# Optimization experiments

Hardware: AMD Instinct MI355X
Metric: run time of the kernel (lower is better)

## Reference

```python
import jax, jax.numpy as jnp
import numpy as np

N_NODES = 100000


def gcn_conv(x, edge_src, edge_dst, W, b):
    # PyG GCNConv: h = x @ W; add self-loops; symmetric normalization; scatter-add; + bias
    n = x.shape[0]
    h = x @ W  # [N, out]
    loop = jnp.arange(n, dtype=edge_src.dtype)
    src = jnp.concatenate([edge_src, loop])
    dst = jnp.concatenate([edge_dst, loop])
    deg = jax.ops.segment_sum(jnp.ones_like(dst, dtype=h.dtype), dst, num_segments=n)
    dinv = jnp.where(deg > 0, jax.lax.rsqrt(deg), 0.0)
    norm = dinv[src] * dinv[dst]  # [E+N]
    msg = h[src] * norm[:, None]  # gather + scale
    out = jax.ops.segment_sum(msg, dst, num_segments=n)  # scatter-add
    return out + b


def setup_inputs() -> dict:
    key = jax.random.key(0)
    ks = jax.random.split(key, 12)
    F_in, H, H2, C = 128, 64, 32, 2
    x = jax.random.normal(ks[0], (N_NODES, F_in), dtype=jnp.float32)
    edge_index = jax.random.randint(ks[1], (2, 3200000), 0, N_NODES, dtype=jnp.int64)
    def glorot(k, shape):
        lim = float(np.sqrt(6.0 / (shape[0] + shape[1])))
        return jax.random.uniform(k, shape, jnp.float32, -lim, lim)
    return {
        "x": x,
        "edge_index": edge_index,
        "W1": glorot(ks[2], (F_in, H)), "b1": jnp.zeros((H,), jnp.float32),
        "W2": glorot(ks[3], (H, H)), "b2": jnp.zeros((H,), jnp.float32),
        "Wl1": glorot(ks[4], (H, H2)), "bl1": jnp.zeros((H2,), jnp.float32),
        "Wl2": glorot(ks[5], (H2, C)), "bl2": jnp.zeros((C,), jnp.float32),
    }


def reference(x, edge_index, W1, b1, W2, b2, Wl1, bl1, Wl2, bl2):
    src, dst = edge_index[0], edge_index[1]
    h = gcn_conv(x, src, dst, W1, b1)
    h = jax.nn.relu(h)
    # dropout is identity in eval mode (training=self.training)
    h = gcn_conv(h, src, dst, W2, b2)
    h = h @ Wl1 + bl1
    h = h @ Wl2 + bl2
    return jax.nn.softmax(h, axis=0)
```

## Files before the change

### kernel.cpp

```cpp
#include <hip/hip_runtime.h>

#define F_IN 128
#define NBMAX 512
#define TILE1 8192
#define CAP2 10240

typedef __attribute__((ext_vector_type(8))) short short8;
typedef __attribute__((ext_vector_type(4))) float f32x4;
typedef __attribute__((ext_vector_type(2))) float f32x2;

__device__ __forceinline__ unsigned short f2bf(float f) {
    unsigned u = __float_as_uint(f);
    u += 0x7fffu + ((u >> 16) & 1u);
    return (unsigned short)(u >> 16);
}
__device__ __forceinline__ float bflo(unsigned u) { return __uint_as_float(u << 16); }
__device__ __forceinline__ float bfhi(unsigned u) { return __uint_as_float(u & 0xffff0000u); }

__device__ __forceinline__ unsigned char f2fp8(float f) {
    return (unsigned char)(__builtin_amdgcn_cvt_pk_fp8_f32(f, f, 0, false) & 0xff);
}

__global__ __launch_bounds__(512) void k_cnt(const int* __restrict__ dst, int E,
                                             int* __restrict__ bcnt, int nb) {
    __shared__ int h[NBMAX];
    int t = threadIdx.x;
    for (int i = t; i < nb; i += 512) h[i] = 0;
    __syncthreads();
    int base = blockIdx.x * TILE1;
    int end = min(base + TILE1, E);
    for (int i = base + t; i < end; i += 512)
        atomicAdd(&h[dst[i] >> 8], 1);
    __syncthreads();
    for (int i = t; i < nb; i += 512)
        if (h[i]) atomicAdd(&bcnt[i], h[i]);
}

__global__ __launch_bounds__(512) void k_bscan1(const int* __restrict__ bcnt,
                                                int* __restrict__ boff,
                                                int* __restrict__ cursor, int nb) {
    __shared__ int part[512];
    int t = threadIdx.x;
    int v = (t < nb) ? bcnt[t] : 0;
    part[t] = v;
    __syncthreads();
    for (int d = 1; d < 512; d <<= 1) {
        int u = (t >= d) ? part[t - d] : 0;
        __syncthreads();
        part[t] += u;
        __syncthreads();
    }
    if (t < nb) { boff[t] = part[t] - v; cursor[t] = part[t] - v; }
    if (t == 511) boff[nb] = part[511];
}

__global__ __launch_bounds__(1024) void k_part1(const int* __restrict__ src,
                                                const int* __restrict__ dst,
                                                int* __restrict__ cursor,
                                                unsigned* __restrict__ ebuf,
                                                int E, int nb) {
    __shared__ unsigned staged[TILE1];
    __shared__ unsigned short sbuck[TILE1];
    __shared__ int hist[NBMAX], lbase[NBMAX], lcur[NBMAX], gbase[NBMAX];
    int t = threadIdx.x;
    for (int i = t; i < nb; i += 1024) hist[i] = 0;
    __syncthreads();
    int base = blockIdx.x * TILE1;
    int end = min(base + TILE1, E);
    for (int i = base + t; i < end; i += 1024)
        atomicAdd(&hist[dst[i] >> 8], 1);
    __syncthreads();
    if (t < 64) {
        int carry = 0;
        for (int c = 0; c < (nb + 63) / 64; ++c) {
            int idx = c * 64 + t;
            int v = (idx < nb) ? hist[idx] : 0;
            int inc = v;
            for (int d = 1; d < 64; d <<= 1) {
                int u = __shfl_up(inc, d, 64);
                if (t >= d) inc += u;
            }
            if (idx < nb) { int ex = carry + inc - v; lbase[idx] = ex; lcur[idx] = ex; }
            carry += __shfl(inc, 63, 64);
        }
    }
    __syncthreads();
    for (int i = t; i < nb; i += 1024)
        gbase[i] = hist[i] ? atomicAdd(&cursor[i], hist[i]) : 0;
    for (int i = base + t; i < end; i += 1024) {
        int d = dst[i];
        int b = d >> 8;
        int r = atomicAdd(&lcur[b], 1);
        staged[r] = ((unsigned)src[i] << 8) | (unsigned)(d & 255);
        sbuck[r] = (unsigned short)b;
    }
    __syncthreads();
    int cnt = end - base;
    for (int i = t; i < cnt; i += 1024) {
        int b = sbuck[i];
        ebuf[gbase[b] + (i - lbase[b])] = staged[i];
    }
}

__global__ __launch_bounds__(1024) void k_part2(const unsigned* __restrict__ ebuf,
                                                const int* __restrict__ boff,
                                                int* __restrict__ csr,
                                                int* __restrict__ offs,
                                                float* __restrict__ dinv, int n) {
    __shared__ unsigned staged[CAP2];
    __shared__ int hist[256], lcur[256];
    int t = threadIdx.x;
    int b = blockIdx.x;
    int beg = boff[b], end = boff[b + 1];
    int cnt = end - beg;
    if (t < 256) hist[t] = 0;
    __syncthreads();
    for (int i = beg + t; i < end; i += 1024)
        atomicAdd(&hist[ebuf[i] & 255u], 1);
    __syncthreads();
    if (t < 64) {
        int carry = 0;
        for (int c = 0; c < 4; ++c) {
            int idx = c * 64 + t;
            int v = hist[idx];
            int inc = v;
            for (int d = 1; d < 64; d <<= 1) {
                int u = __shfl_up(inc, d, 64);
                if (t >= d) inc += u;
            }
            int ex = carry + inc - v;
            lcur[idx] = ex;
            int node = b * 256 + idx;
            if (node <= n) offs[node] = beg + ex;
            if (node < n) dinv[node] = rsqrtf((float)(v + 1));
            carry += __shfl(inc, 63, 64);
        }
    }
    __syncthreads();
    if (cnt <= CAP2) {
        for (int i = beg + t; i < end; i += 1024) {
            unsigned e = ebuf[i];
            int r = atomicAdd(&lcur[(int)(e & 255u)], 1);
            staged[r] = e >> 8;
        }
        __syncthreads();
        for (int i = t; i < cnt; i += 1024)
            csr[beg + i] = (int)staged[i];
    } else {
        for (int i = beg + t; i < end; i += 1024) {
            unsigned e = ebuf[i];
            int r = atomicAdd(&lcur[(int)(e & 255u)], 1);
            csr[beg + r] = (int)(e >> 8);
        }
    }
}

__global__ __launch_bounds__(256) void k_wfold(const float* __restrict__ W2,
                                               const float* __restrict__ b2,
                                               const float* __restrict__ Wl1,
                                               const float* __restrict__ bl1,
                                               const float* __restrict__ Wl2,
                                               const float* __restrict__ bl2,
                                               float* __restrict__ Wfold,
                                               float* __restrict__ bconst) {
    __shared__ float Wc[64][2];
    __shared__ float bc0[2];
    int t = threadIdx.x;
    if (t < 128) {
        int k = t >> 1, c = t & 1;
        float s = 0.f;
        for (int m = 0; m < 32; ++m) s += Wl1[k * 32 + m] * Wl2[m * 2 + c];
        Wc[k][c] = s;
    } else if (t < 130) {
        int c = t - 128;
        float s = bl2[c];
        for (int m = 0; m < 32; ++m) s += bl1[m] * Wl2[m * 2 + c];
        bc0[c] = s;
    }
    __syncthreads();
    if (t < 128) {
        int k = t >> 1, c = t & 1;
        float s = 0.f;
        for (int j = 0; j < 64; ++j) s += W2[k * 64 + j] * Wc[j][c];
        Wfold[k * 2 + c] = s;
    } else if (t < 130) {
        int c = t - 128;
        float s = bc0[c];
        for (int j = 0; j < 64; ++j) s += b2[j] * Wc[j][c];
        bconst[c] = s;
    }
}

template<int K, bool INBF16>
__global__ __launch_bounds__(256) void k_gemm_mfma(const void* __restrict__ Xv,
                                                   const float* __restrict__ W,
                                                   const float* __restrict__ dinv,
                                                   unsigned* __restrict__ G, int n) {
    constexpr int AST = K + 8;
    __shared__ unsigned short A_lds[64 * AST];
    __shared__ unsigned short Wt_lds[64 * AST];
    __shared__ unsigned char C8[64 * 68];
    int t = threadIdx.x;
    int base = blockIdx.x * 64;

    for (int idx = t; idx < K * 64; idx += 256) {
        int k = idx >> 6, nn = idx & 63;
        Wt_lds[nn * AST + k] = f2bf(W[idx]);
    }
    if (!INBF16) {
        const f32x4* X4 = (const f32x4*)Xv;
        constexpr int F4 = K / 4;
        for (int idx = t; idx < 64 * F4; idx += 256) {
            int row = idx / F4, c4 = idx % F4;
            f32x4 f = {0.f, 0.f, 0.f, 0.f};
            if (base + row < n) f = X4[(size_t)base * F4 + idx];
            unsigned p0 = (unsigned)f2bf(f.x) | ((unsigned)f2bf(f.y) << 16);
            unsigned p1 = (unsigned)f2bf(f.z) | ((unsigned)f2bf(f.w) << 16);
            *(uint2*)&A_lds[row * AST + c4 * 4] = make_uint2(p0, p1);
        }
    } else {
        const unsigned* H32 = (const unsigned*)Xv;
        constexpr int U2 = K / 2;
        for (int idx = t; idx < 64 * U2; idx += 256) {
            int row = idx / U2, c2 = idx % U2;
            unsigned u = 0;
            if (base + row < n) u = H32[(size_t)base * U2 + idx];
            *(unsigned*)&A_lds[row * AST + c2 * 2] = u;
        }
    }
    __syncthreads();

    int lane = t & 63, w = t >> 6;
    int q = lane >> 4, m = lane & 15;
    f32x4 acc0 = {0,0,0,0}, acc1 = {0,0,0,0}, acc2 = {0,0,0,0}, acc3 = {0,0,0,0};
    const unsigned short* arow = &A_lds[(16 * w + m) * AST + q * 8];
#pragma unroll
    for (int s = 0; s < K / 32; ++s) {
        short8 a  = *(const short8*)(arow + s * 32);
        short8 w0 = *(const short8*)&Wt_lds[ m       * AST + s * 32 + q * 8];
        short8 w1 = *(const short8*)&Wt_lds[(16 + m) * AST + s * 32 + q * 8];
        short8 w2 = *(const short8*)&Wt_lds[(32 + m) * AST + s * 32 + q * 8];
        short8 w3 = *(const short8*)&Wt_lds[(48 + m) * AST + s * 32 + q * 8];
        acc0 = __builtin_amdgcn_mfma_f32_16x16x32_bf16(a, w0, acc0, 0, 0, 0);
        acc1 = __builtin_amdgcn_mfma_f32_16x16x32_bf16(a, w1, acc1, 0, 0, 0);
        acc2 = __builtin_amdgcn_mfma_f32_16x16x32_bf16(a, w2, acc2, 0, 0, 0);
        acc3 = __builtin_amdgcn_mfma_f32_16x16x32_bf16(a, w3, acc3, 0, 0, 0);
    }
    float dv[4];
#pragma unroll
    for (int r = 0; r < 4; ++r) {
        int node = base + 16 * w + q * 4 + r;
        dv[r] = (node < n) ? dinv[node] : 0.f;
    }
#pragma unroll
    for (int r = 0; r < 4; ++r) {
        int row = 16 * w + q * 4 + r;
        C8[row * 68 + m]      = f2fp8(acc0[r] * dv[r]);
        C8[row * 68 + 16 + m] = f2fp8(acc1[r] * dv[r]);
        C8[row * 68 + 32 + m] = f2fp8(acc2[r] * dv[r]);
        C8[row * 68 + 48 + m] = f2fp8(acc3[r] * dv[r]);
    }
    __syncthreads();
    for (int idx = t; idx < 1024; idx += 256) {
        int row = idx >> 4, c4 = idx & 15;
        int node = base + row;
        if (node < n) G[(size_t)node * 16 + c4] = *(const unsigned*)&C8[row * 68 + c4 * 4];
    }
}

__global__ __launch_bounds__(256) void k_gfold(const int* __restrict__ csr,
                                               const int* __restrict__ offs,
                                               const unsigned* __restrict__ G,
                                               const float* __restrict__ dinv,
                                               const float* __restrict__ bias,
                                               const float* __restrict__ Wfold,
                                               float2* __restrict__ P, int n) {
    int w = (blockIdx.x * 256 + threadIdx.x) >> 6;
    if (w >= n) return;
    int lane = threadIdx.x & 63;
    int g = lane >> 4, sl = lane & 15;
    float a0 = 0.f, a1 = 0.f, a2 = 0.f, a3 = 0.f;
    {
        unsigned u = G[(size_t)w * 16 + sl];
        if (g != 0) u = 0u;
        f32x2 lo = __builtin_amdgcn_cvt_pk_f32_fp8((int)u, false);
        f32x2 hi = __builtin_amdgcn_cvt_pk_f32_fp8((int)u, true);
        a0 += lo.x; a1 += lo.y; a2 += hi.x; a3 += hi.y;
    }
    int beg = offs[w], end = offs[w + 1];
    int e = beg;
    int c0 = 0, c1 = 0, c2 = 0, c3 = 0;
    if (e + 16 <= end) {
        c0 = csr[e + g];      c1 = csr[e + 4 + g];
        c2 = csr[e + 8 + g];  c3 = csr[e + 12 + g];
    }
    while (e + 16 <= end) {
        unsigned u0 = G[(size_t)c0 * 16 + sl];
        unsigned u1 = G[(size_t)c1 * 16 + sl];
        unsigned u2 = G[(size_t)c2 * 16 + sl];
        unsigned u3 = G[(size_t)c3 * 16 + sl];
        int ne = e + 16;
        if (ne + 16 <= end) {
            c0 = csr[ne + g];      c1 = csr[ne + 4 + g];
            c2 = csr[ne + 8 + g];  c3 = csr[ne + 12 + g];
        }
        f32x2 p;
        p = __builtin_amdgcn_cvt_pk_f32_fp8((int)u0, false); a0 += p.x; a1 += p.y;
        p = __builtin_amdgcn_cvt_pk_f32_fp8((int)u0, true);  a2 += p.x; a3 += p.y;
        p = __builtin_amdgcn_cvt_pk_f32_fp8((int)u1, false); a0 += p.x; a1 += p.y;
        p = __builtin_amdgcn_cvt_pk_f32_fp8((int)u1, true);  a2 += p.x; a3 += p.y;
        p = __builtin_amdgcn_cvt_pk_f32_fp8((int)u2, false); a0 += p.x; a1 += p.y;
        p = __builtin_amdgcn_cvt_pk_f32_fp8((int)u2, true);  a2 += p.x; a3 += p.y;
        p = __builtin_amdgcn_cvt_pk_f32_fp8((int)u3, false); a0 += p.x; a1 += p.y;
        p = __builtin_amdgcn_cvt_pk_f32_fp8((int)u3, true);  a2 += p.x; a3 += p.y;
        e = ne;
    }
    for (; e + 4 <= end; e += 4) {
        int c = csr[e + g];
        unsigned u = G[(size_t)c * 16 + sl];
        f32x2 lo = __builtin_amdgcn_cvt_pk_f32_fp8((int)u, false);
        f32x2 hi = __builtin_amdgcn_cvt_pk_f32_fp8((int)u, true);
        a0 += lo.x; a1 += lo.y; a2 += hi.x; a3 += hi.y;
    }
    int rem = end - e;
    if (rem > 0) {
        int c = csr[(g < rem) ? (e + g) : e];
        unsigned u = G[(size_t)c * 16 + sl];
        if (g >= rem) u = 0u;
        f32x2 lo = __builtin_amdgcn_cvt_pk_f32_fp8((int)u, false);
        f32x2 hi = __builtin_amdgcn_cvt_pk_f32_fp8((int)u, true);
        a0 += lo.x; a1 += lo.y; a2 += hi.x; a3 += hi.y;
    }
    a0 += __shfl_xor(a0, 16, 64); a1 += __shfl_xor(a1, 16, 64);
    a2 += __shfl_xor(a2, 16, 64); a3 += __shfl_xor(a3, 16, 64);
    a0 += __shfl_xor(a0, 32, 64); a1 += __shfl_xor(a1, 32, 64);
    a2 += __shfl_xor(a2, 32, 64); a3 += __shfl_xor(a3, 32, 64);
    float d = dinv[w];
    float4 bb = ((const float4*)bias)[sl];
    float v0 = fmaxf(fmaf(a0, d, bb.x), 0.f);
    float v1 = fmaxf(fmaf(a1, d, bb.y), 0.f);
    float v2 = fmaxf(fmaf(a2, d, bb.z), 0.f);
    float v3 = fmaxf(fmaf(a3, d, bb.w), 0.f);
    float4 wa = ((const float4*)Wfold)[2 * sl];
    float4 wb = ((const float4*)Wfold)[2 * sl + 1];
    float px = v0 * wa.x + v1 * wa.z + v2 * wb.x + v3 * wb.z;
    float py = v0 * wa.y + v1 * wa.w + v2 * wb.y + v3 * wb.w;
    px += __shfl_xor(px, 1, 64); py += __shfl_xor(py, 1, 64);
    px += __shfl_xor(px, 2, 64); py += __shfl_xor(py, 2, 64);
    px += __shfl_xor(px, 4, 64); py += __shfl_xor(py, 4, 64);
    px += __shfl_xor(px, 8, 64); py += __shfl_xor(py, 8, 64);
    if (lane == 0) P[w] = make_float2(px * d, py * d);
}

__global__ __launch_bounds__(256) void k_gather2(const int* __restrict__ csr,
                                                 const int* __restrict__ offs,
                                                 const float2* __restrict__ P,
                                                 const float* __restrict__ dinv,
                                                 const float* __restrict__ bconst,
                                                 float* __restrict__ logits, int n) {
    int w = (blockIdx.x * 256 + threadIdx.x) >> 4;
    if (w >= n) return;
    int sl = threadIdx.x & 15;
    int beg = offs[w], end = offs[w + 1];
    float ax = 0.f, ay = 0.f;
    for (int i = beg + sl; i < end; i += 16) {
        float2 p = P[csr[i]];
        ax += p.x; ay += p.y;
    }
    ax += __shfl_xor(ax, 1, 64); ay += __shfl_xor(ay, 1, 64);
    ax += __shfl_xor(ax, 2, 64); ay += __shfl_xor(ay, 2, 64);
    ax += __shfl_xor(ax, 4, 64); ay += __shfl_xor(ay, 4, 64);
    ax += __shfl_xor(ax, 8, 64); ay += __shfl_xor(ay, 8, 64);
    if (sl == 0) {
        float2 self = P[w];
        float d = dinv[w];
        logits[w * 2]     = d * (self.x + ax) + bconst[0];
        logits[w * 2 + 1] = d * (self.y + ay) + bconst[1];
    }
}

__global__ __launch_bounds__(256) void k_sm_part(const float* __restrict__ logits,
                                                 float4* __restrict__ partials, int n) {
    __shared__ float r0[256], r1[256];
    int t = threadIdx.x;
    int i = blockIdx.x * 256 + t;
    float l0 = -3.4e38f, l1 = -3.4e38f;
    if (i < n) { l0 = logits[i * 2]; l1 = logits[i * 2 + 1]; }
    r0[t] = l0; r1[t] = l1;
    __syncthreads();
    for (int s = 128; s > 0; s >>= 1) {
        if (t < s) { r0[t] = fmaxf(r0[t], r0[t + s]); r1[t] = fmaxf(r1[t], r1[t + s]); }
        __syncthreads();
    }
    float m0 = r0[0], m1 = r1[0];
    __syncthreads();
    r0[t] = (i < n) ? __expf(l0 - m0) : 0.f;
    r1[t] = (i < n) ? __expf(l1 - m1) : 0.f;
    __syncthreads();
    for (int s = 128; s > 0; s >>= 1) {
        if (t < s) { r0[t] += r0[t + s]; r1[t] += r1[t + s]; }
        __syncthreads();
    }
    if (t == 0) partials[blockIdx.x] = make_float4(m0, r0[0], m1, r1[0]);
}

__global__ __launch_bounds__(512) void k_sm_comb(const float4* __restrict__ partials,
                                                 float4* __restrict__ glob, int nb) {
    __shared__ float m0s[512], s0s[512], m1s[512], s1s[512];
    int t = threadIdx.x;
    float4 p = (t < nb) ? partials[t] : make_float4(-3.4e38f, 0.f, -3.4e38f, 0.f);
    m0s[t] = p.x; m1s[t] = p.z;
    __syncthreads();
    for (int s = 256; s > 0; s >>= 1) {
        if (t < s) { m0s[t] = fmaxf(m0s[t], m0s[t + s]); m1s[t] = fmaxf(m1s[t], m1s[t + s]); }
        __syncthreads();
    }
    float M0 = m0s[0], M1 = m1s[0];
    s0s[t] = (t < nb) ? p.y * __expf(p.x - M0) : 0.f;
    s1s[t] = (t < nb) ? p.w * __expf(p.z - M1) : 0.f;
    __syncthreads();
    for (int s = 256; s > 0; s >>= 1) {
        if (t < s) { s0s[t] += s0s[t + s]; s1s[t] += s1s[t + s]; }
        __syncthreads();
    }
    if (t == 0) *glob = make_float4(M0, 1.f / s0s[0], M1, 1.f / s1s[0]);
}

__global__ __launch_bounds__(256) void k_sm_final(const float* __restrict__ logits,
                                                  const float4* __restrict__ glob,
                                                  float* __restrict__ out, int n) {
    int i = blockIdx.x * 256 + threadIdx.x;
    if (i < n) {
        float4 g = *glob;
        out[i * 2]     = __expf(logits[i * 2]     - g.x) * g.y;
        out[i * 2 + 1] = __expf(logits[i * 2 + 1] - g.z) * g.w;
    }
}

extern "C" void kernel_launch(void* const* d_in, const int* in_sizes, int n_in,
                              void* d_out, int out_size, void* d_ws, size_t ws_size,
                              hipStream_t stream) {
    const float* x   = (const float*)d_in[0];
    const int*   ei  = (const int*)d_in[1];
    const float* W1  = (const float*)d_in[2];
    const float* b1  = (const float*)d_in[3];
    const float* W2  = (const float*)d_in[4];
    const float* b2  = (const float*)d_in[5];
    const float* Wl1 = (const float*)d_in[6];
    const float* bl1 = (const float*)d_in[7];
    const float* Wl2 = (const float*)d_in[8];
    const float* bl2 = (const float*)d_in[9];
    float* out = (float*)d_out;

    int N = in_sizes[0] / F_IN;
    int E = in_sizes[1] / 2;
    const int* esrc = ei;
    const int* edst = ei + E;

    int nbuck = (N + 255) / 256;

    char* ws = (char*)d_ws;
    size_t off = 0;
    auto alloc = [&](size_t bytes) { void* p = ws + off; off += (bytes + 255) & ~(size_t)255; return p; };
    int*            bcnt   = (int*)alloc((size_t)NBMAX * 4);
    int*            boff   = (int*)alloc((size_t)(NBMAX + 1) * 4);
    int*            cursor = (int*)alloc((size_t)NBMAX * 4);
    float*          dinv   = (float*)alloc((size_t)N * 4);
    int*            offs   = (int*)alloc((size_t)(N + 1) * 4);
    int*            csr    = (int*)alloc((size_t)E * 4);
    unsigned*       ebuf   = (unsigned*)alloc((size_t)E * 4);
    unsigned*       gbuf   = (unsigned*)alloc((size_t)N * 64);
    float*          Wfold  = (float*)alloc(64 * 2 * 4);
    float*          bconst = (float*)alloc(2 * 4);
    float2*         P      = (float2*)alloc((size_t)N * 8);
    float*          logits = (float*)alloc((size_t)N * 2 * 4);
    float4*         smpart = (float4*)alloc((size_t)NBMAX * 16);
    float4*         smglob = (float4*)alloc(16);

    hipMemsetAsync(bcnt, 0, NBMAX * sizeof(int), stream);

    int tiles = (E + TILE1 - 1) / TILE1;
    int mb = (N + 63) / 64;
    int wb = (N * 64 + 255) / 256;
    int qb = (N * 16 + 255) / 256;
    int nb = (N + 255) / 256;

    k_cnt<<<tiles, 512, 0, stream>>>(edst, E, bcnt, nbuck);
    k_bscan1<<<1, 512, 0, stream>>>(bcnt, boff, cursor, nbuck);
    k_part1<<<tiles, 1024, 0, stream>>>(esrc, edst, cursor, ebuf, E, nbuck);
    k_part2<<<nbuck, 1024, 0, stream>>>(ebuf, boff, csr, offs, dinv, N);

    k_wfold<<<1, 256, 0, stream>>>(W2, b2, Wl1, bl1, Wl2, bl2, Wfold, bconst);

    k_gemm_mfma<128, false><<<mb, 256, 0, stream>>>(x, W1, dinv, gbuf, N);

    k_gfold<<<wb, 256, 0, stream>>>(csr, offs, gbuf, dinv, b1, Wfold, P, N);

    k_gather2<<<qb, 256, 0, stream>>>(csr, offs, P, dinv, bconst, logits, N);

    k_sm_part<<<nb, 256, 0, stream>>>(logits, smpart, N);
    k_sm_comb<<<1, 512, 0, stream>>>(smpart, smglob, nb);
    k_sm_final<<<nb, 256, 0, stream>>>(logits, smglob, out, N);
}
```

Measured before the change: 255.5 us.

## Eliminate scan, weight-fold and softmax-combine launches; deepen gather unrolling

Removes the separate bucket-scan kernel by having part1 scan the bucket counts itself and part2 sum its own prefix. Folds the weight-fold computation into block 0 of the GEMM, and merges softmax combine into the final kernel using an online max/sum reduction per block. Deepens the neighbor gather loop in gfold to 8 outstanding loads, with 32-bit address arithmetic. This cuts launch and serialization overhead at the cost of redundant per-block reductions.

```diff
diff --git a/kernel.cpp b/kernel.cpp
--- a/kernel.cpp
+++ b/kernel.cpp
@@ -14,11 +14,14 @@
     u += 0x7fffu + ((u >> 16) & 1u);
     return (unsigned short)(u >> 16);
 }
-__device__ __forceinline__ float bflo(unsigned u) { return __uint_as_float(u << 16); }
-__device__ __forceinline__ float bfhi(unsigned u) { return __uint_as_float(u & 0xffff0000u); }
 
 __device__ __forceinline__ unsigned char f2fp8(float f) {
     return (unsigned char)(__builtin_amdgcn_cvt_pk_fp8_f32(f, f, 0, false) & 0xff);
+}
+
+__device__ __forceinline__ unsigned ldG(const unsigned* __restrict__ G,
+                                        unsigned c, unsigned sl) {
+    return *(const unsigned*)((const char*)G + ((c << 6) + (sl << 2)));
 }
 
 __global__ __launch_bounds__(512) void k_cnt(const int* __restrict__ dst, int E,
@@ -36,32 +39,15 @@
         if (h[i]) atomicAdd(&bcnt[i], h[i]);
 }
 
-__global__ __launch_bounds__(512) void k_bscan1(const int* __restrict__ bcnt,
-                                                int* __restrict__ boff,
-                                                int* __restrict__ cursor, int nb) {
-    __shared__ int part[512];
-    int t = threadIdx.x;
-    int v = (t < nb) ? bcnt[t] : 0;
-    part[t] = v;
-    __syncthreads();
-    for (int d = 1; d < 512; d <<= 1) {
-        int u = (t >= d) ? part[t - d] : 0;
-        __syncthreads();
-        part[t] += u;
-        __syncthreads();
-    }
-    if (t < nb) { boff[t] = part[t] - v; cursor[t] = part[t] - v; }
-    if (t == 511) boff[nb] = part[511];
-}
-
 __global__ __launch_bounds__(1024) void k_part1(const int* __restrict__ src,
                                                 const int* __restrict__ dst,
+                                                const int* __restrict__ bcnt,
                                                 int* __restrict__ cursor,
                                                 unsigned* __restrict__ ebuf,
                                                 int E, int nb) {
     __shared__ unsigned staged[TILE1];
     __shared__ unsigned short sbuck[TILE1];
-    __shared__ int hist[NBMAX], lbase[NBMAX], lcur[NBMAX], gbase[NBMAX];
+    __shared__ int hist[NBMAX], lbase[NBMAX], lcur[NBMAX], gbase[NBMAX], boffL[NBMAX];
     int t = threadIdx.x;
     for (int i = t; i < nb; i += 1024) hist[i] = 0;
     __syncthreads();
@@ -71,22 +57,29 @@
         atomicAdd(&hist[dst[i] >> 8], 1);
     __syncthreads();
     if (t < 64) {
-        int carry = 0;
+        int carry = 0, carry2 = 0;
         for (int c = 0; c < (nb + 63) / 64; ++c) {
             int idx = c * 64 + t;
-            int v = (idx < nb) ? hist[idx] : 0;
-            int inc = v;
+            int v  = (idx < nb) ? hist[idx] : 0;
+            int v2 = (idx < nb) ? bcnt[idx] : 0;
+            int inc = v, inc2 = v2;
             for (int d = 1; d < 64; d <<= 1) {
-                int u = __shfl_up(inc, d, 64);
-                if (t >= d) inc += u;
+                int u  = __shfl_up(inc,  d, 64);
+                int u2 = __shfl_up(inc2, d, 64);
+                if (t >= d) { inc += u; inc2 += u2; }
             }
-            if (idx < nb) { int ex = carry + inc - v; lbase[idx] = ex; lcur[idx] = ex; }
-            carry += __shfl(inc, 63, 64);
+            if (idx < nb) {
+                int ex = carry + inc - v;
+                lbase[idx] = ex; lcur[idx] = ex;
+                boffL[idx] = carry2 + inc2 - v2;
+            }
+            carry  += __shfl(inc,  63, 64);
+            carry2 += __shfl(inc2, 63, 64);
         }
     }
     __syncthreads();
     for (int i = t; i < nb; i += 1024)
-        gbase[i] = hist[i] ? atomicAdd(&cursor[i], hist[i]) : 0;
+        gbase[i] = boffL[i] + (hist[i] ? atomicAdd(&cursor[i], hist[i]) : 0);
     for (int i = base + t; i < end; i += 1024) {
         int d = dst[i];
         int b = d >> 8;
@@ -103,18 +96,26 @@
 }
 
 __global__ __launch_bounds__(1024) void k_part2(const unsigned* __restrict__ ebuf,
-                                                const int* __restrict__ boff,
+                                                const int* __restrict__ bcnt,
                                                 int* __restrict__ csr,
                                                 int* __restrict__ offs,
                                                 float* __restrict__ dinv, int n) {
     __shared__ unsigned staged[CAP2];
     __shared__ int hist[256], lcur[256];
+    __shared__ int begS;
     int t = threadIdx.x;
     int b = blockIdx.x;
-    int beg = boff[b], end = boff[b + 1];
+    if (t < 256) hist[t] = 0;
+    if (t >= 256 && t < 320) {
+        int sl = t - 256;
+        int s = 0;
+        for (int i = sl; i < b; i += 64) s += bcnt[i];
+        for (int m = 32; m >= 1; m >>= 1) s += __shfl_xor(s, m, 64);
+        if (sl == 0) begS = s;
+    }
+    __syncthreads();
+    int beg = begS, end = begS + bcnt[b];
     int cnt = end - beg;
-    if (t < 256) hist[t] = 0;
-    __syncthreads();
     for (int i = beg + t; i < end; i += 1024)
         atomicAdd(&hist[ebuf[i] & 255u], 1);
     __syncthreads();
@@ -155,53 +156,53 @@
     }
 }
 
-__global__ __launch_bounds__(256) void k_wfold(const float* __restrict__ W2,
-                                               const float* __restrict__ b2,
-                                               const float* __restrict__ Wl1,
-                                               const float* __restrict__ bl1,
-                                               const float* __restrict__ Wl2,
-                                               const float* __restrict__ bl2,
-                                               float* __restrict__ Wfold,
-                                               float* __restrict__ bconst) {
-    __shared__ float Wc[64][2];
-    __shared__ float bc0[2];
-    int t = threadIdx.x;
-    if (t < 128) {
-        int k = t >> 1, c = t & 1;
-        float s = 0.f;
-        for (int m = 0; m < 32; ++m) s += Wl1[k * 32 + m] * Wl2[m * 2 + c];
-        Wc[k][c] = s;
-    } else if (t < 130) {
-        int c = t - 128;
-        float s = bl2[c];
-        for (int m = 0; m < 32; ++m) s += bl1[m] * Wl2[m * 2 + c];
-        bc0[c] = s;
-    }
-    __syncthreads();
-    if (t < 128) {
-        int k = t >> 1, c = t & 1;
-        float s = 0.f;
-        for (int j = 0; j < 64; ++j) s += W2[k * 64 + j] * Wc[j][c];
-        Wfold[k * 2 + c] = s;
-    } else if (t < 130) {
-        int c = t - 128;
-        float s = bc0[c];
-        for (int j = 0; j < 64; ++j) s += b2[j] * Wc[j][c];
-        bconst[c] = s;
-    }
-}
-
 template<int K, bool INBF16>
 __global__ __launch_bounds__(256) void k_gemm_mfma(const void* __restrict__ Xv,
                                                    const float* __restrict__ W,
                                                    const float* __restrict__ dinv,
-                                                   unsigned* __restrict__ G, int n) {
+                                                   unsigned* __restrict__ G, int n,
+                                                   const float* __restrict__ W2,
+                                                   const float* __restrict__ b2,
+                                                   const float* __restrict__ Wl1,
+                                                   const float* __restrict__ bl1,
+                                                   const float* __restrict__ Wl2,
+                                                   const float* __restrict__ bl2,
+                                                   float* __restrict__ Wfold,
+                                                   float* __restrict__ bconst) {
     constexpr int AST = K + 8;
     __shared__ unsigned short A_lds[64 * AST];
     __shared__ unsigned short Wt_lds[64 * AST];
     __shared__ unsigned char C8[64 * 68];
+    __shared__ float Wc[64][2];
+    __shared__ float bc0[2];
     int t = threadIdx.x;
     int base = blockIdx.x * 64;
+
+    if (blockIdx.x == 0) {
+        if (t < 128) {
+            int k = t >> 1, c = t & 1;
+            float s = 0.f;
+            for (int m = 0; m < 32; ++m) s += Wl1[k * 32 + m] * Wl2[m * 2 + c];
+            Wc[k][c] = s;
+        } else if (t < 130) {
+            int c = t - 128;
+            float s = bl2[c];
+            for (int m = 0; m < 32; ++m) s += bl1[m] * Wl2[m * 2 + c];
+            bc0[c] = s;
+        }
+        __syncthreads();
+        if (t < 128) {
+            int k = t >> 1, c = t & 1;
+            float s = 0.f;
+            for (int j = 0; j < 64; ++j) s += W2[k * 64 + j] * Wc[j][c];
+            Wfold[k * 2 + c] = s;
+        } else if (t < 130) {
+            int c = t - 128;
+            float s = bc0[c];
+            for (int j = 0; j < 64; ++j) s += b2[j] * Wc[j][c];
+            bconst[c] = s;
+        }
+    }
 
     for (int idx = t; idx < K * 64; idx += 256) {
         int k = idx >> 6, nn = idx & 63;
@@ -278,59 +279,82 @@
     int w = (blockIdx.x * 256 + threadIdx.x) >> 6;
     if (w >= n) return;
     int lane = threadIdx.x & 63;
-    int g = lane >> 4, sl = lane & 15;
-    float a0 = 0.f, a1 = 0.f, a2 = 0.f, a3 = 0.f;
+    unsigned g = (unsigned)lane >> 4, sl = (unsigned)lane & 15u;
+    f32x2 A01 = {0.f, 0.f}, A23 = {0.f, 0.f};
     {
-        unsigned u = G[(size_t)w * 16 + sl];
+        unsigned u = ldG(G, (unsigned)w, sl);
         if (g != 0) u = 0u;
-        f32x2 lo = __builtin_amdgcn_cvt_pk_f32_fp8((int)u, false);
-        f32x2 hi = __builtin_amdgcn_cvt_pk_f32_fp8((int)u, true);
-        a0 += lo.x; a1 += lo.y; a2 += hi.x; a3 += hi.y;
+        A01 += __builtin_amdgcn_cvt_pk_f32_fp8((int)u, false);
+        A23 += __builtin_amdgcn_cvt_pk_f32_fp8((int)u, true);
     }
     int beg = offs[w], end = offs[w + 1];
     int e = beg;
-    int c0 = 0, c1 = 0, c2 = 0, c3 = 0;
-    if (e + 16 <= end) {
-        c0 = csr[e + g];      c1 = csr[e + 4 + g];
-        c2 = csr[e + 8 + g];  c3 = csr[e + 12 + g];
-    }
-    while (e + 16 <= end) {
-        unsigned u0 = G[(size_t)c0 * 16 + sl];
-        unsigned u1 = G[(size_t)c1 * 16 + sl];
-        unsigned u2 = G[(size_t)c2 * 16 + sl];
-        unsigned u3 = G[(size_t)c3 * 16 + sl];
-        int ne = e + 16;
-        if (ne + 16 <= end) {
-            c0 = csr[ne + g];      c1 = csr[ne + 4 + g];
-            c2 = csr[ne + 8 + g];  c3 = csr[ne + 12 + g];
-        }
-        f32x2 p;
-        p = __builtin_amdgcn_cvt_pk_f32_fp8((int)u0, false); a0 += p.x; a1 += p.y;
-        p = __builtin_amdgcn_cvt_pk_f32_fp8((int)u0, true);  a2 += p.x; a3 += p.y;
-        p = __builtin_amdgcn_cvt_pk_f32_fp8((int)u1, false); a0 += p.x; a1 += p.y;
-        p = __builtin_amdgcn_cvt_pk_f32_fp8((int)u1, true);  a2 += p.x; a3 += p.y;
-        p = __builtin_amdgcn_cvt_pk_f32_fp8((int)u2, false); a0 += p.x; a1 += p.y;
-        p = __builtin_amdgcn_cvt_pk_f32_fp8((int)u2, true);  a2 += p.x; a3 += p.y;
-        p = __builtin_amdgcn_cvt_pk_f32_fp8((int)u3, false); a0 += p.x; a1 += p.y;
-        p = __builtin_amdgcn_cvt_pk_f32_fp8((int)u3, true);  a2 += p.x; a3 += p.y;
+    unsigned c0=0,c1=0,c2=0,c3=0,c4=0,c5=0,c6=0,c7=0;
+    if (e + 32 <= end) {
+        c0 = (unsigned)csr[e + g];       c1 = (unsigned)csr[e + 4 + g];
+        c2 = (unsigned)csr[e + 8 + g];   c3 = (unsigned)csr[e + 12 + g];
+        c4 = (unsigned)csr[e + 16 + g];  c5 = (unsigned)csr[e + 20 + g];
+        c6 = (unsigned)csr[e + 24 + g];  c7 = (unsigned)csr[e + 28 + g];
+    }
+    while (e + 32 <= end) {
+        unsigned u0 = ldG(G, c0, sl);
+        unsigned u1 = ldG(G, c1, sl);
+        unsigned u2 = ldG(G, c2, sl);
+        unsigned u3 = ldG(G, c3, sl);
+        unsigned u4 = ldG(G, c4, sl);
+        unsigned u5 = ldG(G, c5, sl);
+        unsigned u6 = ldG(G, c6, sl);
+        unsigned u7 = ldG(G, c7, sl);
+        int ne = e + 32;
+        if (ne + 32 <= end) {
+            c0 = (unsigned)csr[ne + g];       c1 = (unsigned)csr[ne + 4 + g];
+            c2 = (unsigned)csr[ne + 8 + g];   c3 = (unsigned)csr[ne + 12 + g];
+            c4 = (unsigned)csr[ne + 16 + g];  c5 = (unsigned)csr[ne + 20 + g];
+            c6 = (unsigned)csr[ne + 24 + g];  c7 = (unsigned)csr[ne + 28 + g];
+        }
+        A01 += __builtin_amdgcn_cvt_pk_f32_fp8((int)u0, false);
+        A23 += __builtin_amdgcn_cvt_pk_f32_fp8((int)u0, true);
+        A01 += __builtin_amdgcn_cvt_pk_f32_fp8((int)u1, false);
+        A23 += __builtin_amdgcn_cvt_pk_f32_fp8((int)u1, true);
+        A01 += __builtin_amdgcn_cvt_pk_f32_fp8((int)u2, false);
+        A23 += __builtin_amdgcn_cvt_pk_f32_fp8((int)u2, true);
+        A01 += __builtin_amdgcn_cvt_pk_f32_fp8((int)u3, false);
+        A23 += __builtin_amdgcn_cvt_pk_f32_fp8((int)u3, true);
+        A01 += __builtin_amdgcn_cvt_pk_f32_fp8((int)u4, false);
+        A23 += __builtin_amdgcn_cvt_pk_f32_fp8((int)u4, true);
+        A01 += __builtin_amdgcn_cvt_pk_f32_fp8((int)u5, false);
+        A23 += __builtin_amdgcn_cvt_pk_f32_fp8((int)u5, true);
+        A01 += __builtin_amdgcn_cvt_pk_f32_fp8((int)u6, false);
+        A23 += __builtin_amdgcn_cvt_pk_f32_fp8((int)u6, true);
+        A01 += __builtin_amdgcn_cvt_pk_f32_fp8((int)u7, false);
+        A23 += __builtin_amdgcn_cvt_pk_f32_fp8((int)u7, true);
         e = ne;
     }
-    for (; e + 4 <= end; e += 4) {
-        int c = csr[e + g];
-        unsigned u = G[(size_t)c * 16 + sl];
-        f32x2 lo = __builtin_amdgcn_cvt_pk_f32_fp8((int)u, false);
-        f32x2 hi = __builtin_amdgcn_cvt_pk_f32_fp8((int)u, true);
-        a0 += lo.x; a1 += lo.y; a2 += hi.x; a3 += hi.y;
+    for (; e + 8 <= end; e += 8) {
+        unsigned d0 = (unsigned)csr[e + g], d1 = (unsigned)csr[e + 4 + g];
+        unsigned u0 = ldG(G, d0, sl);
+        unsigned u1 = ldG(G, d1, sl);
+        A01 += __builtin_amdgcn_cvt_pk_f32_fp8((int)u0, false);
+        A23 += __builtin_amdgcn_cvt_pk_f32_fp8((int)u0, true);
+        A01 += __builtin_amdgcn_cvt_pk_f32_fp8((int)u1, false);
+        A23 += __builtin_amdgcn_cvt_pk_f32_fp8((int)u1, true);
+    }
+    if (e + 4 <= end) {
+        unsigned d0 = (unsigned)csr[e + g];
+        unsigned u = ldG(G, d0, sl);
+        A01 += __builtin_amdgcn_cvt_pk_f32_fp8((int)u, false);
+        A23 += __builtin_amdgcn_cvt_pk_f32_fp8((int)u, true);
+        e += 4;
     }
     int rem = end - e;
     if (rem > 0) {
-        int c = csr[(g < rem) ? (e + g) : e];
-        unsigned u = G[(size_t)c * 16 + sl];
-        if (g >= rem) u = 0u;
-        f32x2 lo = __builtin_amdgcn_cvt_pk_f32_fp8((int)u, false);
-        f32x2 hi = __builtin_amdgcn_cvt_pk_f32_fp8((int)u, true);
-        a0 += lo.x; a1 += lo.y; a2 += hi.x; a3 += hi.y;
-    }
+        unsigned c = (unsigned)csr[((int)g < rem) ? (e + (int)g) : e];
+        unsigned u = ldG(G, c, sl);
+        if ((int)g >= rem) u = 0u;
+        A01 += __builtin_amdgcn_cvt_pk_f32_fp8((int)u, false);
+        A23 += __builtin_amdgcn_cvt_pk_f32_fp8((int)u, true);
+    }
+    float a0 = A01.x, a1 = A01.y, a2 = A23.x, a3 = A23.y;
     a0 += __shfl_xor(a0, 16, 64); a1 += __shfl_xor(a1, 16, 64);
     a2 += __shfl_xor(a2, 16, 64); a3 += __shfl_xor(a3, 16, 64);
     a0 += __shfl_xor(a0, 32, 64); a1 += __shfl_xor(a1, 32, 64);
@@ -364,7 +388,7 @@
     int beg = offs[w], end = offs[w + 1];
     float ax = 0.f, ay = 0.f;
     for (int i = beg + sl; i < end; i += 16) {
-        float2 p = P[csr[i]];
+        float2 p = *(const float2*)((const char*)P + ((unsigned)csr[i] << 3));
         ax += p.x; ay += p.y;
     }
     ax += __shfl_xor(ax, 1, 64); ay += __shfl_xor(ay, 1, 64);
@@ -404,36 +428,40 @@
     if (t == 0) partials[blockIdx.x] = make_float4(m0, r0[0], m1, r1[0]);
 }
 
-__global__ __launch_bounds__(512) void k_sm_comb(const float4* __restrict__ partials,
-                                                 float4* __restrict__ glob, int nb) {
-    __shared__ float m0s[512], s0s[512], m1s[512], s1s[512];
+__global__ __launch_bounds__(256) void k_sm_final(const float* __restrict__ logits,
+                                                  const float4* __restrict__ partials,
+                                                  float* __restrict__ out, int n, int nbp) {
+    __shared__ float m0s[256], s0s[256], m1s[256], s1s[256];
     int t = threadIdx.x;
-    float4 p = (t < nb) ? partials[t] : make_float4(-3.4e38f, 0.f, -3.4e38f, 0.f);
-    m0s[t] = p.x; m1s[t] = p.z;
-    __syncthreads();
-    for (int s = 256; s > 0; s >>= 1) {
-        if (t < s) { m0s[t] = fmaxf(m0s[t], m0s[t + s]); m1s[t] = fmaxf(m1s[t], m1s[t + s]); }
+    float m0 = -3.4e38f, s0 = 0.f, m1 = -3.4e38f, s1 = 0.f;
+    for (int i = t; i < nbp; i += 256) {
+        float4 p = partials[i];
+        float M = fmaxf(m0, p.x);
+        s0 = s0 * __expf(m0 - M) + p.y * __expf(p.x - M); m0 = M;
+        M = fmaxf(m1, p.z);
+        s1 = s1 * __expf(m1 - M) + p.w * __expf(p.z - M); m1 = M;
+    }
+    m0s[t] = m0; s0s[t] = s0; m1s[t] = m1; s1s[t] = s1;
+    __syncthreads();
+    for (int s = 128; s > 0; s >>= 1) {
+        if (t < s) {
+            float Ma = m0s[t], Mb = m0s[t + s];
+            float M = fmaxf(Ma, Mb);
+            s0s[t] = s0s[t] * __expf(Ma - M) + s0s[t + s] * __expf(Mb - M);
+            m0s[t] = M;
+            Ma = m1s[t]; Mb = m1s[t + s];
+            M = fmaxf(Ma, Mb);
+            s1s[t] = s1s[t] * __expf(Ma - M) + s1s[t + s] * __expf(Mb - M);
+            m1s[t] = M;
+        }
         __syncthreads();
     }
-    float M0 = m0s[0], M1 = m1s[0];
-    s0s[t] = (t < nb) ? p.y * __expf(p.x - M0) : 0.f;
-    s1s[t] = (t < nb) ? p.w * __expf(p.z - M1) : 0.f;
-    __syncthreads();
-    for (int s = 256; s > 0; s >>= 1) {
-        if (t < s) { s0s[t] += s0s[t + s]; s1s[t] += s1s[t + s]; }
-        __syncthreads();
-    }
-    if (t == 0) *glob = make_float4(M0, 1.f / s0s[0], M1, 1.f / s1s[0]);
-}
-
-__global__ __launch_bounds__(256) void k_sm_final(const float* __restrict__ logits,
-                                                  const float4* __restrict__ glob,
-                                                  float* __restrict__ out, int n) {
-    int i = blockIdx.x * 256 + threadIdx.x;
+    float M0 = m0s[0], inv0 = 1.f / s0s[0];
+    float M1 = m1s[0], inv1 = 1.f / s1s[0];
+    int i = blockIdx.x * 256 + t;
     if (i < n) {
-        float4 g = *glob;
-        out[i * 2]     = __expf(logits[i * 2]     - g.x) * g.y;
-        out[i * 2 + 1] = __expf(logits[i * 2 + 1] - g.z) * g.w;
+        out[i * 2]     = __expf(logits[i * 2]     - M0) * inv0;
+        out[i * 2 + 1] = __expf(logits[i * 2 + 1] - M1) * inv1;
     }
 }
 
@@ -463,7 +491,6 @@
     size_t off = 0;
     auto alloc = [&](size_t bytes) { void* p = ws + off; off += (bytes + 255) & ~(size_t)255; return p; };
     int*            bcnt   = (int*)alloc((size_t)NBMAX * 4);
-    int*            boff   = (int*)alloc((size_t)(NBMAX + 1) * 4);
     int*            cursor = (int*)alloc((size_t)NBMAX * 4);
     float*          dinv   = (float*)alloc((size_t)N * 4);
     int*            offs   = (int*)alloc((size_t)(N + 1) * 4);
@@ -475,9 +502,8 @@
     float2*         P      = (float2*)alloc((size_t)N * 8);
     float*          logits = (float*)alloc((size_t)N * 2 * 4);
     float4*         smpart = (float4*)alloc((size_t)NBMAX * 16);
-    float4*         smglob = (float4*)alloc(16);
-
-    hipMemsetAsync(bcnt, 0, NBMAX * sizeof(int), stream);
+
+    hipMemsetAsync(bcnt, 0, 2 * NBMAX * sizeof(int), stream);
 
     int tiles = (E + TILE1 - 1) / TILE1;
     int mb = (N + 63) / 64;
@@ -486,19 +512,17 @@
     int nb = (N + 255) / 256;
 
     k_cnt<<<tiles, 512, 0, stream>>>(edst, E, bcnt, nbuck);
-    k_bscan1<<<1, 512, 0, stream>>>(bcnt, boff, cursor, nbuck);
-    k_part1<<<tiles, 1024, 0, stream>>>(esrc, edst, cursor, ebuf, E, nbuck);
-    k_part2<<<nbuck, 1024, 0, stream>>>(ebuf, boff, csr, offs, dinv, N);
-
-    k_wfold<<<1, 256, 0, stream>>>(W2, b2, Wl1, bl1, Wl2, bl2, Wfold, bconst);
-
-    k_gemm_mfma<128, false><<<mb, 256, 0, stream>>>(x, W1, dinv, gbuf, N);
+    k_part1<<<tiles, 1024, 0, stream>>>(esrc, edst, bcnt, cursor, ebuf, E, nbuck);
+    k_part2<<<nbuck, 1024, 0, stream>>>(ebuf, bcnt, csr, offs, dinv, N);
+
+    k_gemm_mfma<128, false><<<mb, 256, 0, stream>>>(x, W1, dinv, gbuf, N,
+                                                    W2, b2, Wl1, bl1, Wl2, bl2,
+                                                    Wfold, bconst);
 
     k_gfold<<<wb, 256, 0, stream>>>(csr, offs, gbuf, dinv, b1, Wfold, P, N);
 
     k_gather2<<<qb, 256, 0, stream>>>(csr, offs, P, dinv, bconst, logits, N);
 
     k_sm_part<<<nb, 256, 0, stream>>>(logits, smpart, N);
-    k_sm_comb<<<1, 512, 0, stream>>>(smpart, smglob, nb);
-    k_sm_final<<<nb, 256, 0, stream>>>(logits, smglob, out, N);
-}
+    k_sm_final<<<nb, 256, 0, stream>>>(logits, smpart, out, N, nb);
+}
```

Result: faster. 246.6 us (-3.5%).
